# Optimization experiments

Measured on AMD Instinct MI355X. Metric: run time of the kernel, lower is better.

Reference implementation:

```python
import jax, jax.numpy as jnp
import numpy as np

LAYER_SIZES = [4096, 8192, 8192, 4096, 1024]
BATCH = 4096
SCARCITY = 0.05


def setup_inputs() -> dict:
    key = jax.random.key(0)
    ks = jax.random.split(key, 5)
    inp = {"x": jax.random.normal(ks[0], (LAYER_SIZES[0], BATCH), dtype=jnp.float32)}
    for i in range(4):
        out_d, in_d = LAYER_SIZES[i + 1], LAYER_SIZES[i]
        # uniform(-0.1, 0.1) mirrors the repo's weight_initialization(a=-0.1, b=0.1)
        inp[f"W{i}"] = jax.random.uniform(ks[i + 1], (out_d, in_d), dtype=jnp.float32,
                                          minval=-0.1, maxval=0.1)
        inp[f"thr{i}"] = jnp.ones((out_d,), dtype=jnp.float32)  # starting_threshold = 1.0
    return inp


def _kwta(x, thr, k):
    # x: [out, batch]; per-column k-winners-take-all on (x - thr)
    act = x - thr[:, None]
    kth = jax.lax.top_k(act.T, k)[0][:, -1]          # [batch] k-th largest per column
    mask = act >= kth[None, :]
    return jnp.where(mask, x, jnp.zeros_like(x))


def reference(x, W0, W1, W2, W3, thr0, thr1, thr2, thr3):
    Ws = [W0, W1, W2, W3]
    thrs = [thr0, thr1, thr2, thr3]
    n_layers = len(Ws)
    for i in range(n_layers):
        x = Ws[i] @ x                                 # [out_i, batch]
        if i < n_layers - 1:
            x = jax.nn.relu(x)
        k = int(SCARCITY * Ws[i].shape[0])
        x = _kwta(x, thrs[i], k)
    return jax.nn.softmax(x, axis=0)                  # output_activation over features
```

## Files before the change

### kernel.cpp

```cpp
#include <hip/hip_runtime.h>

typedef _Float16 f16x8 __attribute__((ext_vector_type(8)));
typedef _Float16 f16x4 __attribute__((ext_vector_type(4)));
typedef float f32x4 __attribute__((ext_vector_type(4)));

#define NB 4096

__device__ __forceinline__ void gload16(const void* g, void* l) {
    __builtin_amdgcn_global_load_lds(
        (const __attribute__((address_space(1))) unsigned int*)g,
        (__attribute__((address_space(3))) unsigned int*)l, 16, 0, 0);
}

__global__ __launch_bounds__(256) void tsplit_kernel(const float* __restrict__ X,
                                                     _Float16* __restrict__ Oh,
                                                     _Float16* __restrict__ Ol) {
    __shared__ float t[64][65];
    const int f0 = blockIdx.x * 64, b0 = blockIdx.y * 64;
    const int tid = threadIdx.x;
    const int jj = tid & 63, i0 = tid >> 6;
#pragma unroll
    for (int p = 0; p < 16; ++p) {
        int i = p * 4 + i0;
        t[i][jj] = X[(size_t)(f0 + i) * NB + b0 + jj];
    }
    __syncthreads();
#pragma unroll
    for (int p = 0; p < 16; ++p) {
        int b = p * 4 + i0;
        float v = t[jj][b];
        size_t idx = (size_t)(b0 + b) * 4096 + f0 + jj;
        _Float16 h = (_Float16)v;
        Oh[idx] = h;
        Ol[idx] = (_Float16)((v - (float)h) * 2048.0f);
    }
}

__global__ __launch_bounds__(256) void splitw_kernel(const float* __restrict__ W,
                                                     _Float16* __restrict__ Wh,
                                                     _Float16* __restrict__ Wl, long n4) {
    long i = (long)blockIdx.x * 256 + threadIdx.x;
    const long stride = (long)gridDim.x * 256;
    for (; i < n4; i += stride) {
        float4 w = ((const float4*)W)[i];
        float vs[4] = {w.x, w.y, w.z, w.w};
        f16x4 h, l;
#pragma unroll
        for (int j = 0; j < 4; ++j) {
            _Float16 hh = (_Float16)vs[j];
            h[j] = hh;
            l[j] = (_Float16)((vs[j] - (float)hh) * 2048.0f);
        }
        ((f16x4*)Wh)[i] = h;
        ((f16x4*)Wl)[i] = l;
    }
}

__global__ __launch_bounds__(512, 2) void gemm3p_kernel(
    const _Float16* __restrict__ Ah, const _Float16* __restrict__ Al,
    const _Float16* __restrict__ Bh, const _Float16* __restrict__ Bl,
    float* __restrict__ C, int K, int M, int do_relu) {
    __shared__ __align__(16) char lds[3][49152];

    const int tid = threadIdx.x;
    const int gx = gridDim.x;
    int bid = blockIdx.y * gx + blockIdx.x;
    const int SC = gx < 16 ? gx : 16;
    const int SR = 256 / SC;
    const int nsc = gx / SC;
    const int s = bid >> 8, w = bid & 255;
    const int col0 = ((s % nsc) * SC + (w % SC)) * 256;
    const int row0 = ((s / nsc) * SR + (w / SC)) * 128;

    const int wid = tid >> 6, lane = tid & 63;
    const int wm = wid >> 2, wn = wid & 3;
    const int lr = lane & 15;
    const int rdoff = (((lane >> 4) ^ ((lane >> 1) & 3)) << 4);

    f32x4 acc[4][4] = {};
    f32x4 accx[4][4] = {};

    const int srow = tid >> 2;
    const int scl = (tid & 3) ^ ((tid >> 3) & 3);
    const size_t sk = (size_t)K;
    const _Float16* gA_h = Ah + (size_t)(row0 + srow) * sk + scl * 8;
    const _Float16* gA_l = Al + (size_t)(row0 + srow) * sk + scl * 8;
    const _Float16* gB_h0 = Bh + (size_t)(col0 + srow) * sk + scl * 8;
    const _Float16* gB_h1 = Bh + (size_t)(col0 + 128 + srow) * sk + scl * 8;
    const _Float16* gB_l0 = Bl + (size_t)(col0 + srow) * sk + scl * 8;
    const _Float16* gB_l1 = Bl + (size_t)(col0 + 128 + srow) * sk + scl * 8;
    const int ldsA = tid * 16;

#define STAGE_G0(Lb, go) { gload16(gA_h + go, (Lb) + ldsA); gload16(gA_l + go, (Lb) + 8192 + ldsA); }
#define STAGE_G1(Lb, go) { gload16(gB_h0 + go, (Lb) + 16384 + ldsA); gload16(gB_h1 + go, (Lb) + 24576 + ldsA); }
#define STAGE_G2(Lb, go) { gload16(gB_l0 + go, (Lb) + 32768 + ldsA); gload16(gB_l1 + go, (Lb) + 40960 + ldsA); }

    const int NT = K / 32;
    {
        STAGE_G0(lds[0], 0); STAGE_G1(lds[0], 0); STAGE_G2(lds[0], 0);
        STAGE_G0(lds[1], 32); STAGE_G1(lds[1], 32); STAGE_G2(lds[1], 32);
    }

    for (int t = 0; t < NT; ++t) {
        if (t < NT - 1) {
            asm volatile("s_waitcnt vmcnt(6)" ::: "memory");
        } else {
            asm volatile("s_waitcnt vmcnt(0)" ::: "memory");
        }
        __builtin_amdgcn_s_barrier();
        asm volatile("" ::: "memory");

        const char* Lb = lds[t % 3];
        char* Ls = lds[(t + 2) % 3];
        const bool do_stage = (t + 2 < NT);
        const size_t go = (size_t)(t + 2) * 32;

        const char* sAh_ = Lb;
        const char* sAl_ = Lb + 8192;
        const char* sBh_ = Lb + 16384;
        const char* sBl_ = Lb + 32768;

        f16x8 ah[4], al[4], bh[4], bl[4];
#define READG(i)                                                              \
    {                                                                         \
        const int ra = wm * 64 + (i)*16 + lr;                                 \
        const int rb = wn * 64 + (i)*16 + lr;                                 \
        ah[i] = *(const f16x8*)(sAh_ + ra * 64 + rdoff);                      \
        al[i] = *(const f16x8*)(sAl_ + ra * 64 + rdoff);                      \
        bh[i] = *(const f16x8*)(sBh_ + rb * 64 + rdoff);                      \
        bl[i] = *(const f16x8*)(sBl_ + rb * 64 + rdoff);                      \
    }
#define CL(mi, ni)                                                                               \
    {                                                                                            \
        acc[mi][ni] = __builtin_amdgcn_mfma_f32_16x16x32_f16(ah[mi], bh[ni], acc[mi][ni], 0, 0, 0);  \
        accx[mi][ni] = __builtin_amdgcn_mfma_f32_16x16x32_f16(ah[mi], bl[ni], accx[mi][ni], 0, 0, 0); \
        accx[mi][ni] = __builtin_amdgcn_mfma_f32_16x16x32_f16(al[mi], bh[ni], accx[mi][ni], 0, 0, 0); \
    }
        READG(0)
        READG(1)
        asm volatile("s_waitcnt lgkmcnt(4)" ::: "memory");
        __builtin_amdgcn_sched_barrier(0);
        __builtin_amdgcn_s_setprio(1);
        CL(0, 0)
        __builtin_amdgcn_s_setprio(0);

        READG(2)
        if (do_stage) STAGE_G0(Ls, go);
        asm volatile("s_waitcnt lgkmcnt(4)" ::: "memory");
        __builtin_amdgcn_sched_barrier(0);
        __builtin_amdgcn_s_setprio(1);
        CL(0, 1) CL(1, 0) CL(1, 1)
        __builtin_amdgcn_s_setprio(0);

        READG(3)
        if (do_stage) STAGE_G1(Ls, go);
        asm volatile("s_waitcnt lgkmcnt(4)" ::: "memory");
        __builtin_amdgcn_sched_barrier(0);
        __builtin_amdgcn_s_setprio(1);
        CL(0, 2) CL(1, 2) CL(2, 0) CL(2, 1) CL(2, 2)
        __builtin_amdgcn_s_setprio(0);

        if (do_stage) STAGE_G2(Ls, go);
        asm volatile("s_waitcnt lgkmcnt(0)" ::: "memory");
        __builtin_amdgcn_sched_barrier(0);
        __builtin_amdgcn_s_setprio(1);
        CL(0, 3) CL(1, 3) CL(2, 3) CL(3, 0) CL(3, 1) CL(3, 2) CL(3, 3)
        __builtin_amdgcn_s_setprio(0);
#undef READG
#undef CL
    }
#undef STAGE_G0
#undef STAGE_G1
#undef STAGE_G2

#pragma unroll
    for (int mi = 0; mi < 4; ++mi)
#pragma unroll
        for (int ni = 0; ni < 4; ++ni) {
            int colx = col0 + wn * 64 + ni * 16 + lr;
            int rowb = row0 + wm * 64 + mi * 16 + ((lane >> 4) << 2);
#pragma unroll
            for (int r = 0; r < 4; ++r) {
                float v = acc[mi][ni][r] + accx[mi][ni][r] * (1.0f / 2048.0f);
                if (do_relu) v = fmaxf(v, 0.0f);
                C[(size_t)(rowb + r) * M + colx] = v;
            }
        }
}

template <int CNT, bool SOFTMAX>
__global__ __launch_bounds__(256) void kwta_kernel(const float* __restrict__ Cin,
                                                   const float* __restrict__ thr,
                                                   _Float16* __restrict__ Oh,
                                                   _Float16* __restrict__ Ol,
                                                   float* __restrict__ outT, int M, int k) {
    const int row = blockIdx.x, tid = threadIdx.x;
    const float* rp = Cin + (size_t)row * M;
    unsigned uv[CNT];
    float xv[CNT];
#pragma unroll
    for (int i = 0; i < CNT; ++i) {
        int col = i * 256 + tid;
        float x = rp[col];
        float a = x - thr[col];
        unsigned b = __float_as_uint(a);
        uv[i] = (b & 0x80000000u) ? ~b : (b | 0x80000000u);
        xv[i] = x;
    }
    __shared__ int hist[256];
    __shared__ unsigned sel_s;
    __shared__ int kk_s;
    unsigned prefix = 0;
    int kk = k;
#pragma unroll
    for (int pass = 0; pass < 4; ++pass) {
        const int shift = 24 - pass * 8;
        hist[tid] = 0;
        __syncthreads();
#pragma unroll
        for (int i = 0; i < CNT; ++i) {
            bool ok = (pass == 0) || ((uv[i] >> (shift + 8)) == prefix);
            if (ok) atomicAdd(&hist[(uv[i] >> shift) & 255], 1);
        }
        __syncthreads();
        for (int off = 1; off < 256; off <<= 1) {
            int v = hist[tid] + ((tid + off < 256) ? hist[tid + off] : 0);
            __syncthreads();
            hist[tid] = v;
            __syncthreads();
        }
        if (hist[tid] >= kk && (tid == 255 || hist[tid + 1] < kk)) {
            sel_s = (unsigned)tid;
            kk_s = kk - ((tid == 255) ? 0 : hist[tid + 1]);
        }
        __syncthreads();
        prefix = (prefix << 8) | sel_s;
        kk = kk_s;
        __syncthreads();
    }
    const unsigned kth = prefix;
    if (!SOFTMAX) {
#pragma unroll
        for (int i = 0; i < CNT; ++i) {
            int col = i * 256 + tid;
            float v = (uv[i] >= kth) ? xv[i] : 0.0f;
            size_t idx = (size_t)row * M + col;
            _Float16 h = (_Float16)v;
            Oh[idx] = h;
            Ol[idx] = (_Float16)((v - (float)h) * 2048.0f);
        }
    } else {
        float vals[CNT];
        float m = -3.4e38f;
#pragma unroll
        for (int i = 0; i < CNT; ++i) {
            float v = (uv[i] >= kth) ? xv[i] : 0.0f;
            vals[i] = v;
            m = fmaxf(m, v);
        }
        for (int off = 32; off; off >>= 1) m = fmaxf(m, __shfl_xor(m, off));
        __shared__ float redm[4];
        if ((tid & 63) == 0) redm[tid >> 6] = m;
        __syncthreads();
        m = fmaxf(fmaxf(redm[0], redm[1]), fmaxf(redm[2], redm[3]));
        float s = 0.0f, e[CNT];
#pragma unroll
        for (int i = 0; i < CNT; ++i) {
            e[i] = expf(vals[i] - m);
            s += e[i];
        }
        for (int off = 32; off; off >>= 1) s += __shfl_xor(s, off);
        __shared__ float reds[4];
        if ((tid & 63) == 0) reds[tid >> 6] = s;
        __syncthreads();
        s = reds[0] + reds[1] + reds[2] + reds[3];
        float inv = 1.0f / s;
#pragma unroll
        for (int i = 0; i < CNT; ++i)
            outT[(size_t)(i * 256 + tid) * NB + row] = e[i] * inv;
    }
}

extern "C" void kernel_launch(void* const* d_in, const int* in_sizes, int n_in,
                              void* d_out, int out_size, void* d_ws, size_t ws_size,
                              hipStream_t stream) {
    const float* x = (const float*)d_in[0];
    const float* W0 = (const float*)d_in[1];
    const float* thr0 = (const float*)d_in[2];
    const float* W1 = (const float*)d_in[3];
    const float* thr1 = (const float*)d_in[4];
    const float* W2 = (const float*)d_in[5];
    const float* thr2 = (const float*)d_in[6];
    const float* W3 = (const float*)d_in[7];
    const float* thr3 = (const float*)d_in[8];
    float* out = (float*)d_out;

    char* ws = (char*)d_ws;
    size_t off = 0;
    auto alloc = [&](size_t bytes) {
        void* p = ws + off;
        off += (bytes + 255) & ~(size_t)255;
        return p;
    };
    _Float16* Wh = (_Float16*)alloc((size_t)8192 * 8192 * 2);
    _Float16* Wl = (_Float16*)alloc((size_t)8192 * 8192 * 2);
    _Float16* Xh = (_Float16*)alloc((size_t)4096 * 8192 * 2);
    _Float16* Xl = (_Float16*)alloc((size_t)4096 * 8192 * 2);
    _Float16* Yh = (_Float16*)alloc((size_t)4096 * 8192 * 2);
    _Float16* Yl = (_Float16*)alloc((size_t)4096 * 8192 * 2);
    float* C32 = (float*)alloc((size_t)4096 * 8192 * 4);

    tsplit_kernel<<<dim3(64, 64), 256, 0, stream>>>(x, Xh, Xl);

    splitw_kernel<<<4096, 256, 0, stream>>>(W0, Wh, Wl, (long)8192 * 4096 / 4);
    gemm3p_kernel<<<dim3(8192 / 256, NB / 128), 512, 0, stream>>>(Xh, Xl, Wh, Wl, C32, 4096, 8192, 1);
    kwta_kernel<32, false><<<NB, 256, 0, stream>>>(C32, thr0, Yh, Yl, nullptr, 8192, 409);

    splitw_kernel<<<4096, 256, 0, stream>>>(W1, Wh, Wl, (long)8192 * 8192 / 4);
    gemm3p_kernel<<<dim3(8192 / 256, NB / 128), 512, 0, stream>>>(Yh, Yl, Wh, Wl, C32, 8192, 8192, 1);
    kwta_kernel<32, false><<<NB, 256, 0, stream>>>(C32, thr1, Xh, Xl, nullptr, 8192, 409);

    splitw_kernel<<<4096, 256, 0, stream>>>(W2, Wh, Wl, (long)4096 * 8192 / 4);
    gemm3p_kernel<<<dim3(4096 / 256, NB / 128), 512, 0, stream>>>(Xh, Xl, Wh, Wl, C32, 8192, 4096, 1);
    kwta_kernel<16, false><<<NB, 256, 0, stream>>>(C32, thr2, Yh, Yl, nullptr, 4096, 204);

    splitw_kernel<<<4096, 256, 0, stream>>>(W3, Wh, Wl, (long)1024 * 4096 / 4);
    gemm3p_kernel<<<dim3(1024 / 256, NB / 128), 512, 0, stream>>>(Yh, Yl, Wh, Wl, C32, 4096, 1024, 0);
    kwta_kernel<4, true><<<NB, 256, 0, stream>>>(C32, thr3, nullptr, nullptr, out, 1024, 51);
}
```

Baseline: 3.256 ms.

## Shrink GEMM tile to 128x128 with 256 threads and double buffering

Reduces the 3-pass fp16 GEMM block tile from 128x256 with 512 threads and triple-buffered LDS to 128x128 with 256 threads and double-buffered LDS. The tile-swizzle grouping is recomputed for the new grid size. The K-loop now waits for all outstanding global loads each iteration instead of keeping one stage in flight. This lowers LDS use and raises block count, which may help occupancy and tail balance, but it lowers data reuse per block and weakens latency hiding.

Result: slower. 3.362 ms (+3.3%).

```diff
diff --git a/kernel.cpp b/kernel.cpp
--- a/kernel.cpp
+++ b/kernel.cpp
@@ -56,24 +56,25 @@
     }
 }
 
-__global__ __launch_bounds__(512, 2) void gemm3p_kernel(
+__global__ __launch_bounds__(256, 2) void gemm3p_kernel(
     const _Float16* __restrict__ Ah, const _Float16* __restrict__ Al,
     const _Float16* __restrict__ Bh, const _Float16* __restrict__ Bl,
     float* __restrict__ C, int K, int M, int do_relu) {
-    __shared__ __align__(16) char lds[3][49152];
+    __shared__ __align__(16) char lds[2][32768];
 
     const int tid = threadIdx.x;
-    const int gx = gridDim.x;
+    const int gx = gridDim.x, gy = gridDim.y;
     int bid = blockIdx.y * gx + blockIdx.x;
     const int SC = gx < 16 ? gx : 16;
-    const int SR = 256 / SC;
+    int SR = 512 / SC; if (SR > gy) SR = gy;
+    const int W = SC * SR;
     const int nsc = gx / SC;
-    const int s = bid >> 8, w = bid & 255;
-    const int col0 = ((s % nsc) * SC + (w % SC)) * 256;
+    const int s = bid / W, w = bid % W;
+    const int col0 = ((s % nsc) * SC + (w % SC)) * 128;
     const int row0 = ((s / nsc) * SR + (w / SC)) * 128;
 
     const int wid = tid >> 6, lane = tid & 63;
-    const int wm = wid >> 2, wn = wid & 3;
+    const int wm = wid >> 1, wn = wid & 1;
     const int lr = lane & 15;
     const int rdoff = (((lane >> 4) ^ ((lane >> 1) & 3)) << 4);
 
@@ -84,51 +85,44 @@
     const int scl = (tid & 3) ^ ((tid >> 3) & 3);
     const size_t sk = (size_t)K;
     const _Float16* gA_h = Ah + (size_t)(row0 + srow) * sk + scl * 8;
+    const _Float16* gA_h2 = gA_h + 64 * sk;
     const _Float16* gA_l = Al + (size_t)(row0 + srow) * sk + scl * 8;
-    const _Float16* gB_h0 = Bh + (size_t)(col0 + srow) * sk + scl * 8;
-    const _Float16* gB_h1 = Bh + (size_t)(col0 + 128 + srow) * sk + scl * 8;
-    const _Float16* gB_l0 = Bl + (size_t)(col0 + srow) * sk + scl * 8;
-    const _Float16* gB_l1 = Bl + (size_t)(col0 + 128 + srow) * sk + scl * 8;
+    const _Float16* gA_l2 = gA_l + 64 * sk;
+    const _Float16* gB_h = Bh + (size_t)(col0 + srow) * sk + scl * 8;
+    const _Float16* gB_h2 = gB_h + 64 * sk;
+    const _Float16* gB_l = Bl + (size_t)(col0 + srow) * sk + scl * 8;
+    const _Float16* gB_l2 = gB_l + 64 * sk;
     const int ldsA = tid * 16;
 
-#define STAGE_G0(Lb, go) { gload16(gA_h + go, (Lb) + ldsA); gload16(gA_l + go, (Lb) + 8192 + ldsA); }
-#define STAGE_G1(Lb, go) { gload16(gB_h0 + go, (Lb) + 16384 + ldsA); gload16(gB_h1 + go, (Lb) + 24576 + ldsA); }
-#define STAGE_G2(Lb, go) { gload16(gB_l0 + go, (Lb) + 32768 + ldsA); gload16(gB_l1 + go, (Lb) + 40960 + ldsA); }
+#define SA0(Lb, go) { gload16(gA_h + go, (Lb) + ldsA); gload16(gA_h2 + go, (Lb) + 4096 + ldsA); }
+#define SA1(Lb, go) { gload16(gA_l + go, (Lb) + 8192 + ldsA); gload16(gA_l2 + go, (Lb) + 12288 + ldsA); }
+#define SB0(Lb, go) { gload16(gB_h + go, (Lb) + 16384 + ldsA); gload16(gB_h2 + go, (Lb) + 20480 + ldsA); }
+#define SB1(Lb, go) { gload16(gB_l + go, (Lb) + 24576 + ldsA); gload16(gB_l2 + go, (Lb) + 28672 + ldsA); }
 
     const int NT = K / 32;
     {
-        STAGE_G0(lds[0], 0); STAGE_G1(lds[0], 0); STAGE_G2(lds[0], 0);
-        STAGE_G0(lds[1], 32); STAGE_G1(lds[1], 32); STAGE_G2(lds[1], 32);
+        SA0(lds[0], 0) SA1(lds[0], 0) SB0(lds[0], 0) SB1(lds[0], 0)
     }
 
     for (int t = 0; t < NT; ++t) {
-        if (t < NT - 1) {
-            asm volatile("s_waitcnt vmcnt(6)" ::: "memory");
-        } else {
-            asm volatile("s_waitcnt vmcnt(0)" ::: "memory");
-        }
+        asm volatile("s_waitcnt vmcnt(0)" ::: "memory");
         __builtin_amdgcn_s_barrier();
         asm volatile("" ::: "memory");
 
-        const char* Lb = lds[t % 3];
-        char* Ls = lds[(t + 2) % 3];
-        const bool do_stage = (t + 2 < NT);
-        const size_t go = (size_t)(t + 2) * 32;
-
-        const char* sAh_ = Lb;
-        const char* sAl_ = Lb + 8192;
-        const char* sBh_ = Lb + 16384;
-        const char* sBl_ = Lb + 32768;
+        const char* Lb = lds[t & 1];
+        char* Ls = lds[(t + 1) & 1];
+        const bool do_stage = (t + 1 < NT);
+        const size_t go = (size_t)(t + 1) * 32;
 
         f16x8 ah[4], al[4], bh[4], bl[4];
 #define READG(i)                                                              \
     {                                                                         \
         const int ra = wm * 64 + (i)*16 + lr;                                 \
         const int rb = wn * 64 + (i)*16 + lr;                                 \
-        ah[i] = *(const f16x8*)(sAh_ + ra * 64 + rdoff);                      \
-        al[i] = *(const f16x8*)(sAl_ + ra * 64 + rdoff);                      \
-        bh[i] = *(const f16x8*)(sBh_ + rb * 64 + rdoff);                      \
-        bl[i] = *(const f16x8*)(sBl_ + rb * 64 + rdoff);                      \
+        ah[i] = *(const f16x8*)(Lb + ra * 64 + rdoff);                        \
+        al[i] = *(const f16x8*)(Lb + 8192 + ra * 64 + rdoff);                 \
+        bh[i] = *(const f16x8*)(Lb + 16384 + rb * 64 + rdoff);                \
+        bl[i] = *(const f16x8*)(Lb + 24576 + rb * 64 + rdoff);                \
     }
 #define CL(mi, ni)                                                                               \
     {                                                                                            \
@@ -138,6 +132,7 @@
     }
         READG(0)
         READG(1)
+        if (do_stage) SA0(Ls, go)
         asm volatile("s_waitcnt lgkmcnt(4)" ::: "memory");
         __builtin_amdgcn_sched_barrier(0);
         __builtin_amdgcn_s_setprio(1);
@@ -145,7 +140,7 @@
         __builtin_amdgcn_s_setprio(0);
 
         READG(2)
-        if (do_stage) STAGE_G0(Ls, go);
+        if (do_stage) SA1(Ls, go)
         asm volatile("s_waitcnt lgkmcnt(4)" ::: "memory");
         __builtin_amdgcn_sched_barrier(0);
         __builtin_amdgcn_s_setprio(1);
@@ -153,14 +148,14 @@
         __builtin_amdgcn_s_setprio(0);
 
         READG(3)
-        if (do_stage) STAGE_G1(Ls, go);
+        if (do_stage) SB0(Ls, go)
         asm volatile("s_waitcnt lgkmcnt(4)" ::: "memory");
         __builtin_amdgcn_sched_barrier(0);
         __builtin_amdgcn_s_setprio(1);
         CL(0, 2) CL(1, 2) CL(2, 0) CL(2, 1) CL(2, 2)
         __builtin_amdgcn_s_setprio(0);
 
-        if (do_stage) STAGE_G2(Ls, go);
+        if (do_stage) SB1(Ls, go)
         asm volatile("s_waitcnt lgkmcnt(0)" ::: "memory");
         __builtin_amdgcn_sched_barrier(0);
         __builtin_amdgcn_s_setprio(1);
@@ -169,9 +164,10 @@
 #undef READG
 #undef CL
     }
-#undef STAGE_G0
-#undef STAGE_G1
-#undef STAGE_G2
+#undef SA0
+#undef SA1
+#undef SB0
+#undef SB1
 
 #pragma unroll
     for (int mi = 0; mi < 4; ++mi)
@@ -313,18 +309,18 @@
     tsplit_kernel<<<dim3(64, 64), 256, 0, stream>>>(x, Xh, Xl);
 
     splitw_kernel<<<4096, 256, 0, stream>>>(W0, Wh, Wl, (long)8192 * 4096 / 4);
-    gemm3p_kernel<<<dim3(8192 / 256, NB / 128), 512, 0, stream>>>(Xh, Xl, Wh, Wl, C32, 4096, 8192, 1);
+    gemm3p_kernel<<<dim3(8192 / 128, NB / 128), 256, 0, stream>>>(Xh, Xl, Wh, Wl, C32, 4096, 8192, 1);
     kwta_kernel<32, false><<<NB, 256, 0, stream>>>(C32, thr0, Yh, Yl, nullptr, 8192, 409);
 
     splitw_kernel<<<4096, 256, 0, stream>>>(W1, Wh, Wl, (long)8192 * 8192 / 4);
-    gemm3p_kernel<<<dim3(8192 / 256, NB / 128), 512, 0, stream>>>(Yh, Yl, Wh, Wl, C32, 8192, 8192, 1);
+    gemm3p_kernel<<<dim3(8192 / 128, NB / 128), 256, 0, stream>>>(Yh, Yl, Wh, Wl, C32, 8192, 8192, 1);
     kwta_kernel<32, false><<<NB, 256, 0, stream>>>(C32, thr1, Xh, Xl, nullptr, 8192, 409);
 
     splitw_kernel<<<4096, 256, 0, stream>>>(W2, Wh, Wl, (long)4096 * 8192 / 4);
-    gemm3p_kernel<<<dim3(4096 / 256, NB / 128), 512, 0, stream>>>(Xh, Xl, Wh, Wl, C32, 8192, 4096, 1);
+    gemm3p_kernel<<<dim3(4096 / 128, NB / 128), 256, 0, stream>>>(Xh, Xl, Wh, Wl, C32, 8192, 4096, 1);
     kwta_kernel<16, false><<<NB, 256, 0, stream>>>(C32, thr2, Yh, Yl, nullptr, 4096, 204);
 
     splitw_kernel<<<4096, 256, 0, stream>>>(W3, Wh, Wl, (long)1024 * 4096 / 4);
-    gemm3p_kernel<<<dim3(1024 / 256, NB / 128), 512, 0, stream>>>(Yh, Yl, Wh, Wl, C32, 4096, 1024, 0);
+    gemm3p_kernel<<<dim3(1024 / 128, NB / 128), 256, 0, stream>>>(Yh, Yl, Wh, Wl, C32, 4096, 1024, 0);
     kwta_kernel<4, true><<<NB, 256, 0, stream>>>(C32, thr3, nullptr, nullptr, out, 1024, 51);
 }
```
